# Optimization experiments

Measured on AMD Instinct MI355X. Metric: run time of the kernel, lower is better.

Reference implementation:

```python
import jax, jax.numpy as jnp
import numpy as np

U_NODES, V_NODES, N_EDGES = 100000, 50000, 2000000
F_DIM, G_DIM, H_DIM = 32, 32, 8
G_HIDDEN = (64, 32)
F_HIDDEN = (64, 32)
OUT_DIM = 1


def _linear_params(key, din, dout):
    kw, kb = jax.random.split(key)
    lim = 1.0 / np.sqrt(din)
    w = jax.random.uniform(kw, (din, dout), jnp.float32, -lim, lim)
    b = jax.random.uniform(kb, (dout,), jnp.float32, -lim, lim)
    return w, b


def setup_inputs() -> dict:
    key = jax.random.key(0)
    ks = jax.random.split(key, 10)
    u = jax.random.normal(ks[0], (U_NODES, F_DIM), jnp.float32)
    v = jax.random.normal(ks[1], (V_NODES, G_DIM), jnp.float32)
    e_vals = jax.random.normal(ks[2], (N_EDGES, H_DIM), jnp.float32)
    e_src = jax.random.randint(ks[3], (N_EDGES,), 0, V_NODES, jnp.int32)  # V-side index (indices[0])
    e_dst = jax.random.randint(ks[4], (N_EDGES,), 0, U_NODES, jnp.int32)  # U-side index (indices[1])
    g_w1, g_b1 = _linear_params(ks[5], F_DIM + G_DIM + H_DIM, G_HIDDEN[0])
    g_w2, g_b2 = _linear_params(ks[6], G_HIDDEN[0], G_HIDDEN[1])
    f_w1, f_b1 = _linear_params(ks[7], F_DIM + G_HIDDEN[1], F_HIDDEN[0])
    f_w2, f_b2 = _linear_params(ks[8], F_HIDDEN[0], F_HIDDEN[1])
    t_w, t_b = _linear_params(ks[9], F_HIDDEN[1], OUT_DIM)
    return {
        "u": u, "v": v, "e_vals": e_vals, "e_src": e_src, "e_dst": e_dst,
        "g_w1": g_w1, "g_b1": g_b1, "g_w2": g_w2, "g_b2": g_b2,
        "f_w1": f_w1, "f_b1": f_b1, "f_w2": f_w2, "f_b2": f_b2,
        "t_w": t_w, "t_b": t_b,
    }


def reference(u, v, e_vals, e_src, e_dst,
              g_w1, g_b1, g_w2, g_b2,
              f_w1, f_b1, f_w2, f_b2,
              t_w, t_b):
    # gather edge endpoint features -> g MLP (two Linear+ReLU layers)
    edge_in = jnp.concatenate([u[e_dst], v[e_src], e_vals], axis=-1)  # (E, F+G+H)
    h = jax.nn.relu(edge_in @ g_w1 + g_b1)
    h = jax.nn.relu(h @ g_w2 + g_b2)  # (E, D)
    # torch.sparse.sum over dim=-3 (V axis) == segment-sum by the U index
    agg = jax.ops.segment_sum(h, e_dst, num_segments=u.shape[0])  # (U, D)
    # f MLP on concat([u, agg])
    z = jax.nn.relu(jnp.concatenate([u, agg], axis=-1) @ f_w1 + f_b1)
    z = jax.nn.relu(z @ f_w2 + f_b2)
    # tail linear (no relu) + sigmoid
    return jax.nn.sigmoid(z @ t_w + t_b)  # (U, 1)
```

## Files before the change

kernel.cpp:

```cpp
#include <hip/hip_runtime.h>
#include <cstdint>
#include <cstddef>

#define U_NODES 100000
#define V_NODES 50000
#define N_EDGES 2000000
#define NSEG_CAP 25


typedef _Float16 f16x8 __attribute__((ext_vector_type(8)));
typedef _Float16 f16x2 __attribute__((ext_vector_type(2)));
typedef float    f32x4 __attribute__((ext_vector_type(4)));

__device__ __forceinline__ void load8f(const float* __restrict__ p, float* x) {
    const float4* p4 = reinterpret_cast<const float4*>(p);
    float4 a = p4[0], b = p4[1];
    x[0]=a.x; x[1]=a.y; x[2]=a.z; x[3]=a.w;
    x[4]=b.x; x[5]=b.y; x[6]=b.z; x[7]=b.w;
}

__device__ __forceinline__ void load32f(const float* __restrict__ p, float* x) {
    #pragma unroll
    for (int q = 0; q < 4; ++q) load8f(p + 8*q, x + 8*q);
}

__device__ __forceinline__ unsigned pack_bf16x2(float a, float b) {
    unsigned ua = __float_as_uint(a);
    ua = (ua + 0x7FFFu + ((ua >> 16) & 1u)) >> 16;
    unsigned ub = __float_as_uint(b);
    ub = (ub + 0x7FFFu + ((ub >> 16) & 1u)) & 0xFFFF0000u;
    return ua | ub;
}

__device__ __forceinline__ unsigned pk16(float a, float b) {
    union { f16x2 h; unsigned u; } c;
    c.h[0] = (_Float16)a; c.h[1] = (_Float16)b;
    return c.u;
}
__device__ __forceinline__ float f16lo(unsigned w) {
    union { unsigned short u; _Float16 h; } c; c.u = (unsigned short)(w & 0xFFFFu);
    return (float)c.h;
}
__device__ __forceinline__ float f16hi(unsigned w) {
    union { unsigned short u; _Float16 h; } c; c.u = (unsigned short)(w >> 16);
    return (float)c.h;
}
__device__ __forceinline__ f16x8 as_f16x8(uint4 x) {
    union { uint4 u; f16x8 h; } c; c.u = x; return c.h;
}

__device__ __forceinline__ float fdot2f(unsigned a, unsigned b, float c) {
#if defined(__has_builtin) && __has_builtin(__builtin_amdgcn_fdot2)
    union { unsigned u; f16x2 h; } ca, cb; ca.u = a; cb.u = b;
    return __builtin_amdgcn_fdot2(ca.h, cb.h, c, false);
#else
    return c + f16lo(a)*f16lo(b) + f16hi(a)*f16hi(b);
#endif
}


__global__ __launch_bounds__(256) void proj_u_kernel(
    const float* __restrict__ u, const float* __restrict__ g_w1,
    float* __restrict__ A)
{
    int n = blockIdx.x * 256 + threadIdx.x;
    if (n >= U_NODES) return;
    float x[32];
    load32f(u + (size_t)n * 32, x);
    float acc[64];
    #pragma unroll
    for (int j = 0; j < 64; ++j) acc[j] = 0.f;
    #pragma unroll
    for (int i = 0; i < 32; ++i) {
        #pragma unroll
        for (int j = 0; j < 64; ++j) acc[j] += x[i] * g_w1[i*64 + j];
    }
    float4* Ap = reinterpret_cast<float4*>(A + (size_t)n * 64);
    #pragma unroll
    for (int q = 0; q < 16; ++q)
        Ap[q] = make_float4(acc[4*q], acc[4*q+1], acc[4*q+2], acc[4*q+3]);
}

__global__ __launch_bounds__(256) void proj_v_kernel(
    const float* __restrict__ v, const float* __restrict__ g_w1,
    const float* __restrict__ g_b1, float* __restrict__ B)
{
    int n = blockIdx.x * 256 + threadIdx.x;
    if (n >= V_NODES) return;
    float x[32];
    load32f(v + (size_t)n * 32, x);
    float acc[64];
    #pragma unroll
    for (int j = 0; j < 64; ++j) acc[j] = g_b1[j];
    #pragma unroll
    for (int i = 0; i < 32; ++i) {
        #pragma unroll
        for (int j = 0; j < 64; ++j) acc[j] += x[i] * g_w1[(32+i)*64 + j];
    }
    float4* Bp = reinterpret_cast<float4*>(B + (size_t)n * 64);
    #pragma unroll
    for (int q = 0; q < 16; ++q)
        Bp[q] = make_float4(acc[4*q], acc[4*q+1], acc[4*q+2], acc[4*q+3]);
}


__global__ __launch_bounds__(256) void rank_kernel(
    const int* __restrict__ e_dst, int* __restrict__ deg, int* __restrict__ rank)
{
    int e = blockIdx.x * 256 + threadIdx.x;
    if (e >= N_EDGES) return;
    rank[e] = atomicAdd(&deg[e_dst[e]], 1);
}

__global__ __launch_bounds__(256) void scan_block_kernel(
    const int* __restrict__ deg, int* __restrict__ off, int* __restrict__ aux, int n)
{
    __shared__ int s[256];
    int tid = threadIdx.x;
    int i = blockIdx.x * 256 + tid;
    int x = (i < n) ? deg[i] : 0;
    s[tid] = x;
    __syncthreads();
    #pragma unroll
    for (int o = 1; o < 256; o <<= 1) {
        int t = (tid >= o) ? s[tid - o] : 0;
        __syncthreads();
        s[tid] += t;
        __syncthreads();
    }
    if (i < n) off[i + 1] = s[tid];
    if (tid == 255) aux[blockIdx.x] = s[255];
}

__global__ __launch_bounds__(512) void scan_aux_kernel(int* __restrict__ aux, int nA)
{
    __shared__ int s[512];
    int tid = threadIdx.x;
    int x = (tid < nA) ? aux[tid] : 0;
    s[tid] = x;
    __syncthreads();
    #pragma unroll
    for (int o = 1; o < 512; o <<= 1) {
        int t = (tid >= o) ? s[tid - o] : 0;
        __syncthreads();
        s[tid] += t;
        __syncthreads();
    }
    if (tid < nA) aux[tid] = s[tid] - x;
}

__global__ __launch_bounds__(256) void scan_add_kernel(
    int* __restrict__ off, const int* __restrict__ aux, int n)
{
    int i = blockIdx.x * 256 + threadIdx.x;
    if (i == 0) off[0] = 0;
    if (i < n) off[i + 1] += aux[i >> 8];
}

__global__ __launch_bounds__(256) void scatter_kernel(
    const int* __restrict__ e_dst, const int* __restrict__ off,
    const int* __restrict__ rank, int* __restrict__ sorted_eid)
{
    int e = blockIdx.x * 256 + threadIdx.x;
    if (e >= N_EDGES) return;
    int d = e_dst[e];
    sorted_eid[off[d] + rank[e]] = e;
}

__global__ __launch_bounds__(256) void permute_pack_kernel(
    const int* __restrict__ e_dst, const int* __restrict__ e_src,
    const int* __restrict__ rank, const int* __restrict__ off,
    const float* __restrict__ e_vals, unsigned* __restrict__ epk)
{
    int e = blockIdx.x * 256 + threadIdx.x;
    if (e >= N_EDGES) return;
    int d = e_dst[e];
    int pos = off[d] + rank[e];
    float ev[8];
    load8f(e_vals + (size_t)e * 8, ev);
    uint4 w0;
    w0.x = (unsigned)d;
    w0.y = (unsigned)e_src[e];
    w0.z = pk16(ev[0], ev[1]);
    w0.w = pk16(ev[2], ev[3]);
    uint2 w1;
    w1.x = pk16(ev[4], ev[5]);
    w1.y = pk16(ev[6], ev[7]);
    unsigned* dst = epk + (size_t)pos * 8;
    *reinterpret_cast<uint4*>(dst)     = w0;
    *reinterpret_cast<uint2*>(dst + 4) = w1;
}


__global__ __launch_bounds__(256) void edge_reg_kernel(
    const float* __restrict__ A, const float* __restrict__ B,
    const unsigned* __restrict__ epk,
    const float* __restrict__ g_w1, const float* __restrict__ g_w2,
    const float* __restrict__ g_b2, float* __restrict__ agg)
{
    __shared__ unsigned s_w2[32 * 33];
    __shared__ __align__(16) unsigned s_w1e[4 * 64];
    __shared__ int   s_d[256];
    __shared__ int   s_meta[4][64];
    __shared__ float s_agg[4][NSEG_CAP][33];
    __shared__ float pub_val[4][2][32];
    __shared__ int   pub_d[4][2];
    __shared__ int   pub_fl[4][2];
    __shared__ int   s_bprev, s_bnext;

    const int tid = threadIdx.x;
    const long bP = (long)blockIdx.x * 256;

    #pragma unroll
    for (int i = 0; i < 4; ++i) {
        int idx = tid + i * 256;
        int kp = idx >> 5, n = idx & 31;
        s_w2[kp * 33 + n] = pk16(g_w2[(2*kp)*32 + n], g_w2[(2*kp+1)*32 + n]);
    }
    {
        int i2 = tid >> 6, c = tid & 63;
        s_w1e[i2 * 64 + c] = pk16(g_w1[(64 + 2*i2)*64 + c], g_w1[(64 + 2*i2 + 1)*64 + c]);
    }
    if (tid == 0) {
        s_bprev = (bP > 0) ? (int)epk[(size_t)(bP - 1) * 8] : -2;
        s_bnext = (bP + 256 < (long)N_EDGES) ? (int)epk[(size_t)(bP + 256) * 8] : -2;
    }
    __syncthreads();

    const int wv   = tid >> 6;
    const int lane = tid & 63;
    const int lm   = lane & 15;
    const int lg   = lane >> 4;
    const long wP  = bP + wv * 64;

    int dM[4], sM[4];
    unsigned evp[4][4];
    #pragma unroll
    for (int mt = 0; mt < 4; ++mt) {
        long pe = wP + mt*16 + lm;
        if (pe < (long)N_EDGES) {
            const unsigned* ep = epk + (size_t)pe * 8;
            uint4 w0 = *reinterpret_cast<const uint4*>(ep);
            uint2 w1 = *reinterpret_cast<const uint2*>(ep + 4);
            dM[mt] = (int)w0.x; sM[mt] = (int)w0.y;
            evp[mt][0] = w0.z; evp[mt][1] = w0.w; evp[mt][2] = w1.x; evp[mt][3] = w1.y;
        } else {
            dM[mt] = -1; sM[mt] = 0;
            evp[mt][0] = evp[mt][1] = evp[mt][2] = evp[mt][3] = 0;
        }
    }
    if (lg == 0) {
        #pragma unroll
        for (int mt = 0; mt < 4; ++mt) s_d[wv*64 + mt*16 + lm] = dM[mt];
    }
    {
        float* z = &s_agg[wv][0][0];
        for (int i = lane; i < NSEG_CAP * 33; i += 64) z[i] = 0.f;
    }

    uint4 afr[4][2];
    #pragma unroll
    for (int kt = 0; kt < 2; ++kt) {
        float acc[4][8];
        #pragma unroll
        for (int mt = 0; mt < 4; ++mt) {
            if (dM[mt] >= 0) {
                const float4* Ap = reinterpret_cast<const float4*>(A + (size_t)dM[mt]*64 + kt*32 + lg*8);
                const float4* Bp = reinterpret_cast<const float4*>(B + (size_t)sM[mt]*64 + kt*32 + lg*8);
                float4 a0 = Ap[0], a1 = Ap[1], b0 = Bp[0], b1 = Bp[1];
                acc[mt][0] = a0.x + b0.x; acc[mt][1] = a0.y + b0.y;
                acc[mt][2] = a0.z + b0.z; acc[mt][3] = a0.w + b0.w;
                acc[mt][4] = a1.x + b1.x; acc[mt][5] = a1.y + b1.y;
                acc[mt][6] = a1.z + b1.z; acc[mt][7] = a1.w + b1.w;
            } else {
                #pragma unroll
                for (int j = 0; j < 8; ++j) acc[mt][j] = 0.f;
            }
        }
        #pragma unroll
        for (int i2 = 0; i2 < 4; ++i2) {
            uint4 wA = *reinterpret_cast<const uint4*>(&s_w1e[i2*64 + kt*32 + lg*8]);
            uint4 wB = *reinterpret_cast<const uint4*>(&s_w1e[i2*64 + kt*32 + lg*8 + 4]);
            unsigned wp0 = wA.x, wp1 = wA.y, wp2 = wA.z, wp3 = wA.w;
            unsigned wp4 = wB.x, wp5 = wB.y, wp6 = wB.z, wp7 = wB.w;
            #pragma unroll
            for (int mt = 0; mt < 4; ++mt) {
                unsigned e2 = evp[mt][i2];
                acc[mt][0] = fdot2f(e2, wp0, acc[mt][0]);
                acc[mt][1] = fdot2f(e2, wp1, acc[mt][1]);
                acc[mt][2] = fdot2f(e2, wp2, acc[mt][2]);
                acc[mt][3] = fdot2f(e2, wp3, acc[mt][3]);
                acc[mt][4] = fdot2f(e2, wp4, acc[mt][4]);
                acc[mt][5] = fdot2f(e2, wp5, acc[mt][5]);
                acc[mt][6] = fdot2f(e2, wp6, acc[mt][6]);
                acc[mt][7] = fdot2f(e2, wp7, acc[mt][7]);
            }
        }
        #pragma unroll
        for (int mt = 0; mt < 4; ++mt) {
            uint4 w;
            w.x = pk16(fmaxf(acc[mt][0], 0.f), fmaxf(acc[mt][1], 0.f));
            w.y = pk16(fmaxf(acc[mt][2], 0.f), fmaxf(acc[mt][3], 0.f));
            w.z = pk16(fmaxf(acc[mt][4], 0.f), fmaxf(acc[mt][5], 0.f));
            w.w = pk16(fmaxf(acc[mt][6], 0.f), fmaxf(acc[mt][7], 0.f));
            afr[mt][kt] = w;
        }
    }

    f32x4 mac[4][2];
    #pragma unroll
    for (int mt = 0; mt < 4; ++mt) {
        #pragma unroll
        for (int nt = 0; nt < 2; ++nt) {
            mac[mt][nt][0] = 0.f; mac[mt][nt][1] = 0.f;
            mac[mt][nt][2] = 0.f; mac[mt][nt][3] = 0.f;
        }
    }
    #pragma unroll
    for (int kt = 0; kt < 2; ++kt) {
        uint4 bf0, bf1;
        int kp = kt*16 + lg*4;
        bf0.x = s_w2[(kp+0)*33 + lm];      bf1.x = s_w2[(kp+0)*33 + 16 + lm];
        bf0.y = s_w2[(kp+1)*33 + lm];      bf1.y = s_w2[(kp+1)*33 + 16 + lm];
        bf0.z = s_w2[(kp+2)*33 + lm];      bf1.z = s_w2[(kp+2)*33 + 16 + lm];
        bf0.w = s_w2[(kp+3)*33 + lm];      bf1.w = s_w2[(kp+3)*33 + 16 + lm];
        f16x8 b0 = as_f16x8(bf0), b1 = as_f16x8(bf1);
        #pragma unroll
        for (int mt = 0; mt < 4; ++mt) {
            f16x8 a = as_f16x8(afr[mt][kt]);
            mac[mt][0] = __builtin_amdgcn_mfma_f32_16x16x32_f16(a, b0, mac[mt][0], 0, 0, 0);
            mac[mt][1] = __builtin_amdgcn_mfma_f32_16x16x32_f16(a, b1, mac[mt][1], 0, 0, 0);
        }
    }

    asm volatile("s_waitcnt lgkmcnt(0)" ::: "memory");

    int myd = s_d[wv*64 + lane];
    int prevd = (lane > 0) ? s_d[wv*64 + lane - 1] : -2;
    bool headb = (lane == 0) || (myd != prevd);
    unsigned long long mask = __ballot(headb);

    long remaining = (long)N_EDGES - wP;
    int validcnt = remaining >= 64 ? 64 : (remaining < 0 ? 0 : (int)remaining);
    unsigned long long vmask = (validcnt >= 64) ? ~0ull : ((1ull << validcnt) - 1ull);
    int nsegV = (int)__popcll(mask & vmask);

    if (headb && lane < validcnt) {
        int sg = (int)__popcll(mask & ((2ull << lane) - 1ull)) - 1;
        s_meta[wv][sg] = lane;
    }

    float b2a = g_b2[lm], b2b = g_b2[16 + lm];

    #pragma unroll
    for (int mt = 0; mt < 4; ++mt) {
        const int ebase = mt*16 + lg*4;
        float v0[4], v1[4];
        #pragma unroll
        for (int r = 0; r < 4; ++r) {
            v0[r] = fmaxf(mac[mt][0][r] + b2a, 0.f);
            v1[r] = fmaxf(mac[mt][1][r] + b2b, 0.f);
        }
        float cs0 = v0[0], cs1 = v1[0];
        int rstart = 0;
        #pragma unroll
        for (int r = 1; r <= 4; ++r) {
            bool cut = (r == 4) || (((mask >> (ebase + r)) & 1ull) != 0);
            if (cut) {
                int e0 = ebase + rstart;
                int dd = s_d[wv*64 + e0];
                if (dd >= 0) {
                    int sg = (int)__popcll(mask & ((2ull << e0) - 1ull)) - 1;
                    if (sg < NSEG_CAP) {
                        atomicAdd(&s_agg[wv][sg][lm], cs0);
                        atomicAdd(&s_agg[wv][sg][16 + lm], cs1);
                    } else {
                        atomicAdd(agg + (size_t)dd*32 + lm, cs0);
                        atomicAdd(agg + (size_t)dd*32 + 16 + lm, cs1);
                    }
                }
                if (r < 4) { rstart = r; cs0 = v0[r]; cs1 = v1[r]; }
            } else {
                cs0 += v0[r]; cs1 += v1[r];
            }
        }
    }

    asm volatile("s_waitcnt lgkmcnt(0)" ::: "memory");

    int nI = (nsegV - 1 < NSEG_CAP ? nsegV - 1 : NSEG_CAP) - 1;
    for (int it = lane; it < nI * 32; it += 64) {
        int sg = 1 + (it >> 5);
        int c  = it & 31;
        int dd = s_d[wv*64 + s_meta[wv][sg]];
        agg[(size_t)dd*32 + c] = s_agg[wv][sg][c];
    }

    if (lane < 32) {
        int c = lane;
        if (nsegV >= 1) {
            pub_val[wv][0][c] = s_agg[wv][0][c];
            if (c == 0) { pub_d[wv][0] = s_d[wv*64]; pub_fl[wv][0] = 0; }
        } else if (c == 0) { pub_d[wv][0] = -3; pub_fl[wv][0] = 0; }
    } else {
        int c = lane - 32;
        if (nsegV >= 2) {
            int sL = nsegV - 1;
            if (sL < NSEG_CAP) {
                pub_val[wv][1][c] = s_agg[wv][sL][c];
                if (c == 0) { pub_d[wv][1] = s_d[wv*64 + s_meta[wv][sL]]; pub_fl[wv][1] = 0; }
            } else {
                pub_val[wv][1][c] = 0.f;
                if (c == 0) { pub_d[wv][1] = s_d[wv*64 + s_meta[wv][sL]]; pub_fl[wv][1] = 1; }
            }
        } else if (c == 0) { pub_d[wv][1] = -3; pub_fl[wv][1] = 0; }
    }
    __syncthreads();

    if (tid < 32) {
        const int c = tid;
        int firstV = -1, lastV = -1;
        #pragma unroll
        for (int k = 0; k < 8; ++k) {
            int dk = pub_d[k >> 1][k & 1];
            if (dk >= 0) { if (firstV < 0) firstV = k; lastV = k; }
        }
        int k = firstV;
        while (firstV >= 0 && k <= lastV) {
            int dk = pub_d[k >> 1][k & 1];
            if (dk < 0) { ++k; continue; }
            int d0 = dk; int kst = k;
            float s = 0.f; int atm = 0;
            while (k <= lastV) {
                int d2 = pub_d[k >> 1][k & 1];
                if (d2 == d0) {
                    s += pub_val[k >> 1][k & 1][c];
                    atm |= pub_fl[k >> 1][k & 1];
                    ++k;
                } else if (d2 < 0) { ++k; }
                else break;
            }
            bool lo = (kst == firstV) && (s_bprev == d0);
            bool ro = (k > lastV) && (s_bnext == d0);
            float* dst = agg + (size_t)d0*32 + c;
            if (lo || ro || atm) atomicAdd(dst, s);
            else *dst = s;
        }
    }
}


template <bool HAS_A>
__global__ __launch_bounds__(256) void edge_mfma_kernel(
    const float* __restrict__ A, const float* __restrict__ B,
    const float* __restrict__ u, const unsigned* __restrict__ epk,
    const float* __restrict__ g_w1, const float* __restrict__ g_w2,
    const float* __restrict__ g_b2, float* __restrict__ agg)
{
    __shared__ unsigned s_h1[256 * 36];
    __shared__ unsigned s_w2[32 * 33];
    __shared__ int s_d[256];
    __shared__ int s_heads[256];
    __shared__ int s_cnt, s_prevd, s_nextd;

    const int tid = threadIdx.x;
    const long p = (long)blockIdx.x * 256 + tid;

    if (tid == 0) {
        s_cnt = 0;
        long pprev = (long)blockIdx.x * 256 - 1;
        s_prevd = (pprev < 0) ? -2 : (int)epk[(size_t)pprev * 8];
        long pnext = (long)blockIdx.x * 256 + 256;
        s_nextd = (pnext >= N_EDGES) ? -2 : (int)epk[(size_t)pnext * 8];
    }
    #pragma unroll
    for (int i = 0; i < 4; ++i) {
        int idx = tid + i * 256;
        int kp = idx >> 5, n = idx & 31;
        s_w2[kp * 33 + n] = pk16(g_w2[(2*kp)*32 + n], g_w2[(2*kp+1)*32 + n]);
    }

    int d = -1;
    if (p < N_EDGES) {
        const unsigned* ep = epk + (size_t)p * 8;
        uint4 w0 = *reinterpret_cast<const uint4*>(ep);
        uint2 w1 = *reinterpret_cast<const uint2*>(ep + 4);
        d = (int)w0.x;
        int s = (int)w0.y;

        float h1[64];
        if constexpr (HAS_A) {
            const float4* Ap = reinterpret_cast<const float4*>(A + (size_t)d * 64);
            #pragma unroll
            for (int q = 0; q < 16; ++q) {
                float4 a = Ap[q];
                h1[4*q+0] = a.x; h1[4*q+1] = a.y; h1[4*q+2] = a.z; h1[4*q+3] = a.w;
            }
        } else {
            #pragma unroll
            for (int j = 0; j < 64; ++j) h1[j] = 0.f;
            float x[32];
            load32f(u + (size_t)d * 32, x);
            #pragma unroll
            for (int i = 0; i < 32; ++i) {
                #pragma unroll
                for (int j = 0; j < 64; ++j) h1[j] += x[i] * g_w1[i*64 + j];
            }
        }
        {
            const float4* Bp = reinterpret_cast<const float4*>(B + (size_t)s * 64);
            #pragma unroll
            for (int q = 0; q < 16; ++q) {
                float4 b = Bp[q];
                h1[4*q+0] += b.x; h1[4*q+1] += b.y; h1[4*q+2] += b.z; h1[4*q+3] += b.w;
            }
        }
        float ev[8];
        ev[0]=f16lo(w0.z); ev[1]=f16hi(w0.z); ev[2]=f16lo(w0.w); ev[3]=f16hi(w0.w);
        ev[4]=f16lo(w1.x); ev[5]=f16hi(w1.x); ev[6]=f16lo(w1.y); ev[7]=f16hi(w1.y);
        #pragma unroll
        for (int i = 0; i < 8; ++i) {
            #pragma unroll
            for (int j = 0; j < 64; ++j) h1[j] += ev[i] * g_w1[(64+i)*64 + j];
        }
        #pragma unroll
        for (int j = 0; j < 64; ++j) h1[j] = fmaxf(h1[j], 0.f);

        #pragma unroll
        for (int q = 0; q < 8; ++q) {
            uint4 w;
            w.x = pk16(h1[8*q+0], h1[8*q+1]);
            w.y = pk16(h1[8*q+2], h1[8*q+3]);
            w.z = pk16(h1[8*q+4], h1[8*q+5]);
            w.w = pk16(h1[8*q+6], h1[8*q+7]);
            *reinterpret_cast<uint4*>(&s_h1[tid*36 + 4*q]) = w;
        }
    }
    s_d[tid] = d;
    __syncthreads();

    if (p < N_EDGES) {
        int prevd = (tid == 0) ? s_prevd : s_d[tid - 1];
        bool true_head = (prevd != d);
        bool is_head = (tid == 0) || true_head;
        if (is_head) {
            int idx = atomicAdd(&s_cnt, 1);
            s_heads[idx] = tid | (true_head ? 0x10000 : 0);
        }
    }

    const int lane = tid & 63;
    const int wb   = (tid >> 6) * 64;
    const int lg   = lane >> 4;
    const int lm   = lane & 15;

    f32x4 acc[4][2];
    #pragma unroll
    for (int mt = 0; mt < 4; ++mt) {
        #pragma unroll
        for (int nt = 0; nt < 2; ++nt) {
            acc[mt][nt][0] = 0.f; acc[mt][nt][1] = 0.f;
            acc[mt][nt][2] = 0.f; acc[mt][nt][3] = 0.f;
        }
    }
    #pragma unroll
    for (int kt = 0; kt < 2; ++kt) {
        uint4 bf0, bf1;
        int kp = kt*16 + lg*4;
        bf0.x = s_w2[(kp+0)*33 + lm];      bf1.x = s_w2[(kp+0)*33 + 16 + lm];
        bf0.y = s_w2[(kp+1)*33 + lm];      bf1.y = s_w2[(kp+1)*33 + 16 + lm];
        bf0.z = s_w2[(kp+2)*33 + lm];      bf1.z = s_w2[(kp+2)*33 + 16 + lm];
        bf0.w = s_w2[(kp+3)*33 + lm];      bf1.w = s_w2[(kp+3)*33 + 16 + lm];
        f16x8 b0 = as_f16x8(bf0), b1 = as_f16x8(bf1);
        #pragma unroll
        for (int mt = 0; mt < 4; ++mt) {
            uint4 av = *reinterpret_cast<const uint4*>(
                &s_h1[(wb + mt*16 + lm)*36 + kt*16 + lg*4]);
            f16x8 a = as_f16x8(av);
            acc[mt][0] = __builtin_amdgcn_mfma_f32_16x16x32_f16(a, b0, acc[mt][0], 0, 0, 0);
            acc[mt][1] = __builtin_amdgcn_mfma_f32_16x16x32_f16(a, b1, acc[mt][1], 0, 0, 0);
        }
    }
    float b2a = g_b2[lm];
    float b2b = g_b2[16 + lm];
    __syncthreads();

    float* h2f = reinterpret_cast<float*>(s_h1);
    #pragma unroll
    for (int mt = 0; mt < 4; ++mt) {
        #pragma unroll
        for (int r = 0; r < 4; ++r) {
            int row = wb + mt*16 + lg*4 + r;
            h2f[row*36 + lm]      = fmaxf(acc[mt][0][r] + b2a, 0.f);
            h2f[row*36 + 16 + lm] = fmaxf(acc[mt][1][r] + b2b, 0.f);
        }
    }
    __syncthreads();

    const int nseg = s_cnt;
    const int next_d = s_nextd;
    for (int w = tid; w < nseg * 16; w += 256) {
        int seg = w >> 4, cp = w & 15;
        int ent = s_heads[seg];
        int h = ent & 0xFFFF;
        bool thead = (ent & 0x10000) != 0;
        int dd = s_d[h];
        float s0 = 0.f, s1 = 0.f;
        int r = h;
        while (r < 256 && s_d[r] == dd) {
            s0 += h2f[r*36 + 2*cp];
            s1 += h2f[r*36 + 2*cp + 1];
            ++r;
        }
        bool end_complete = (r < 256) || (next_d != dd);
        float* dst = agg + (size_t)dd * 32 + 2 * cp;
        if (thead && end_complete) {
            *reinterpret_cast<float2*>(dst) = make_float2(s0, s1);
        } else {
            atomicAdd(dst + 0, s0);
            atomicAdd(dst + 1, s1);
        }
    }
}


template <bool HAS_A, bool HAS_B>
__global__ __launch_bounds__(256) void edge_sorted_kernel(
    const float* __restrict__ A, const float* __restrict__ B,
    const float* __restrict__ u, const float* __restrict__ v,
    const float* __restrict__ e_vals, const int* __restrict__ e_src,
    const int* __restrict__ e_dst, const int* __restrict__ seid,
    const float* __restrict__ g_w1, const float* __restrict__ g_b1,
    const float* __restrict__ g_w2, const float* __restrict__ g_b2,
    float* __restrict__ agg)
{
    __shared__ unsigned lds_h[256][17];
    __shared__ int lds_d[256];
    __shared__ int lds_heads[256];
    __shared__ int lds_cnt;
    __shared__ int lds_prev_d, lds_next_d;

    const int tid = threadIdx.x;
    const long p = (long)blockIdx.x * 256 + tid;

    if (tid == 0) {
        lds_cnt = 0;
        long pprev = (long)blockIdx.x * 256 - 1;
        lds_prev_d = (pprev < 0) ? -2 : e_dst[seid[pprev]];
        long pnext = (long)blockIdx.x * 256 + 256;
        lds_next_d = (pnext >= N_EDGES) ? -2 : e_dst[seid[pnext]];
    }

    int d = -1;
    if (p < N_EDGES) {
        int eid = seid[p];
        d = e_dst[eid];
        int s = e_src[eid];

        float h1[64];
        if constexpr (HAS_A) {
            const float4* Ap = reinterpret_cast<const float4*>(A + (size_t)d * 64);
            #pragma unroll
            for (int q = 0; q < 16; ++q) {
                float4 a = Ap[q];
                h1[4*q+0] = a.x; h1[4*q+1] = a.y; h1[4*q+2] = a.z; h1[4*q+3] = a.w;
            }
        } else {
            #pragma unroll
            for (int j = 0; j < 64; ++j) h1[j] = 0.f;
            float x[32];
            load32f(u + (size_t)d * 32, x);
            #pragma unroll
            for (int i = 0; i < 32; ++i) {
                #pragma unroll
                for (int j = 0; j < 64; ++j) h1[j] += x[i] * g_w1[i*64 + j];
            }
        }
        if constexpr (HAS_B) {
            const float4* Bp = reinterpret_cast<const float4*>(B + (size_t)s * 64);
            #pragma unroll
            for (int q = 0; q < 16; ++q) {
                float4 b = Bp[q];
                h1[4*q+0] += b.x; h1[4*q+1] += b.y; h1[4*q+2] += b.z; h1[4*q+3] += b.w;
            }
        } else {
            #pragma unroll
            for (int j = 0; j < 64; ++j) h1[j] += g_b1[j];
            float x[32];
            load32f(v + (size_t)s * 32, x);
            #pragma unroll
            for (int i = 0; i < 32; ++i) {
                #pragma unroll
                for (int j = 0; j < 64; ++j) h1[j] += x[i] * g_w1[(32+i)*64 + j];
            }
        }
        float ev[8];
        load8f(e_vals + (size_t)eid * 8, ev);
        #pragma unroll
        for (int i = 0; i < 8; ++i) {
            #pragma unroll
            for (int j = 0; j < 64; ++j) h1[j] += ev[i] * g_w1[(64+i)*64 + j];
        }
        #pragma unroll
        for (int j = 0; j < 64; ++j) h1[j] = fmaxf(h1[j], 0.f);

        float h2[32];
        #pragma unroll
        for (int k = 0; k < 32; ++k) h2[k] = g_b2[k];
        #pragma unroll
        for (int i = 0; i < 64; ++i) {
            #pragma unroll
            for (int k = 0; k < 32; ++k) h2[k] += h1[i] * g_w2[i*32 + k];
        }
        #pragma unroll
        for (int cp = 0; cp < 16; ++cp)
            lds_h[tid][cp] = pack_bf16x2(fmaxf(h2[2*cp], 0.f), fmaxf(h2[2*cp+1], 0.f));
    }
    lds_d[tid] = d;
    __syncthreads();

    if (p < N_EDGES) {
        int prevd = (tid == 0) ? lds_prev_d : lds_d[tid - 1];
        bool true_head = (prevd != d);
        bool is_head = (tid == 0) || true_head;
        if (is_head) {
            int idx = atomicAdd(&lds_cnt, 1);
            lds_heads[idx] = tid | (true_head ? 0x10000 : 0);
        }
    }
    __syncthreads();

    const int nseg = lds_cnt;
    const int next_d = lds_next_d;
    for (int w = tid; w < nseg * 16; w += 256) {
        int seg = w >> 4, cp = w & 15;
        int ent = lds_heads[seg];
        int h = ent & 0xFFFF;
        bool thead = (ent & 0x10000) != 0;
        int dd = lds_d[h];
        float s0 = 0.f, s1 = 0.f;
        int r = h;
        while (r < 256 && lds_d[r] == dd) {
            unsigned x = lds_h[r][cp];
            s0 += __uint_as_float(x << 16);
            s1 += __uint_as_float(x & 0xFFFF0000u);
            ++r;
        }
        bool end_complete = (r < 256) || (next_d != dd);
        float* dst = agg + (size_t)dd * 32 + 2 * cp;
        if (thead && end_complete) {
            *reinterpret_cast<float2*>(dst) = make_float2(s0, s1);
        } else {
            atomicAdd(dst + 0, s0);
            atomicAdd(dst + 1, s1);
        }
    }
}


__global__ __launch_bounds__(256) void node_kernel(
    const float* __restrict__ u, const float* __restrict__ agg,
    const float* __restrict__ f_w1, const float* __restrict__ f_b1,
    const float* __restrict__ f_w2, const float* __restrict__ f_b2,
    const float* __restrict__ t_w, const float* __restrict__ t_b,
    float* __restrict__ out)
{
    int n = blockIdx.x * 256 + threadIdx.x;
    if (n >= U_NODES) return;
    float x[64];
    load32f(u   + (size_t)n * 32, x);
    load32f(agg + (size_t)n * 32, x + 32);
    float z1[64];
    #pragma unroll
    for (int j = 0; j < 64; ++j) z1[j] = f_b1[j];
    #pragma unroll
    for (int i = 0; i < 64; ++i) {
        #pragma unroll
        for (int j = 0; j < 64; ++j) z1[j] += x[i] * f_w1[i*64 + j];
    }
    #pragma unroll
    for (int j = 0; j < 64; ++j) z1[j] = fmaxf(z1[j], 0.f);
    float z2[32];
    #pragma unroll
    for (int k = 0; k < 32; ++k) z2[k] = f_b2[k];
    #pragma unroll
    for (int j = 0; j < 64; ++j) {
        #pragma unroll
        for (int k = 0; k < 32; ++k) z2[k] += z1[j] * f_w2[j*32 + k];
    }
    #pragma unroll
    for (int k = 0; k < 32; ++k) z2[k] = fmaxf(z2[k], 0.f);
    float o = t_b[0];
    #pragma unroll
    for (int k = 0; k < 32; ++k) o += z2[k] * t_w[k];
    out[n] = 1.f / (1.f + expf(-o));
}


__global__ __launch_bounds__(256) void edge_direct_kernel(
    const float* __restrict__ u, const float* __restrict__ v,
    const float* __restrict__ e_vals, const int* __restrict__ e_src,
    const int* __restrict__ e_dst, const float* __restrict__ g_w1,
    const float* __restrict__ g_b1, const float* __restrict__ g_w2,
    const float* __restrict__ g_b2, float* __restrict__ agg)
{
    int e = blockIdx.x * 256 + threadIdx.x;
    if (e >= N_EDGES) return;
    int d = e_dst[e];
    int s = e_src[e];
    float x[72];
    load32f(u + (size_t)d * 32, x);
    load32f(v + (size_t)s * 32, x + 32);
    load8f(e_vals + (size_t)e * 8, x + 64);
    float h1[64];
    #pragma unroll
    for (int j = 0; j < 64; ++j) h1[j] = g_b1[j];
    #pragma unroll
    for (int i = 0; i < 72; ++i) {
        #pragma unroll
        for (int j = 0; j < 64; ++j) h1[j] += x[i] * g_w1[i*64 + j];
    }
    #pragma unroll
    for (int j = 0; j < 64; ++j) h1[j] = fmaxf(h1[j], 0.f);
    float acc2[32];
    #pragma unroll
    for (int k = 0; k < 32; ++k) acc2[k] = g_b2[k];
    #pragma unroll
    for (int i = 0; i < 64; ++i) {
        #pragma unroll
        for (int k = 0; k < 32; ++k) acc2[k] += h1[i] * g_w2[i*32 + k];
    }
    float* aggp = agg + (size_t)d * 32;
    #pragma unroll
    for (int k = 0; k < 32; ++k) atomicAdd(aggp + k, fmaxf(acc2[k], 0.f));
}


static inline size_t align256(size_t x) { return (x + 255) & ~(size_t)255; }

extern "C" void kernel_launch(void* const* d_in, const int* in_sizes, int n_in,
                              void* d_out, int out_size, void* d_ws, size_t ws_size,
                              hipStream_t stream) {
    const float* u      = (const float*)d_in[0];
    const float* v      = (const float*)d_in[1];
    const float* e_vals = (const float*)d_in[2];
    const int*   e_src  = (const int*)  d_in[3];
    const int*   e_dst  = (const int*)  d_in[4];
    const float* g_w1   = (const float*)d_in[5];
    const float* g_b1   = (const float*)d_in[6];
    const float* g_w2   = (const float*)d_in[7];
    const float* g_b2   = (const float*)d_in[8];
    const float* f_w1   = (const float*)d_in[9];
    const float* f_b1   = (const float*)d_in[10];
    const float* f_w2   = (const float*)d_in[11];
    const float* f_b2   = (const float*)d_in[12];
    const float* t_w    = (const float*)d_in[13];
    const float* t_b    = (const float*)d_in[14];
    float* out = (float*)d_out;

    char* wsc = (char*)d_ws;
    const int nChunks = (U_NODES + 255) / 256;
    const int eBlocks = (N_EDGES + 255) / 256;

    const size_t degB  = align256((size_t)U_NODES * 4);
    const size_t offB  = align256((size_t)(U_NODES + 1) * 4);
    const size_t auxB  = align256((size_t)nChunks * 4);
    const size_t aggB  = align256((size_t)U_NODES * 32 * 4);
    const size_t e4B   = align256((size_t)N_EDGES * 4);
    const size_t epkB  = align256((size_t)N_EDGES * 32);
    const size_t bB    = align256((size_t)V_NODES * 64 * 4);
    const size_t aB    = align256((size_t)U_NODES * 64 * 4);

    size_t o = 0;
    size_t oDeg = o; o += degB;
    size_t oOff = o; o += offB;
    size_t oAux = o; o += auxB;
    size_t oAgg = o; o += aggB;
    size_t baseNeed = o;

    size_t oEp = o;  o += epkB;
    size_t oBn = o;  o += bB;
    size_t needT2r = o + e4B;
    size_t oAn = o;  o += aB;
    size_t needT1 = o;

    size_t o3 = baseNeed;
    size_t oSeid = o3; o3 += e4B;
    size_t needT4 = o3 + e4B;
    size_t oB3 = o3;   o3 += bB;
    size_t oA3 = o3;   o3 += aB;
    size_t needT3 = o3;

    int* deg   = (int*)(wsc + oDeg);
    int* off   = (int*)(wsc + oOff);
    int* aux   = (int*)(wsc + oAux);
    float* agg = (float*)(wsc + oAgg);

    if (ws_size >= needT2r) {
        const bool hasA = (ws_size >= needT1);
        unsigned* epk = (unsigned*)(wsc + oEp);
        float* B   = (float*)(wsc + oBn);
        float* A   = hasA ? (float*)(wsc + oAn) : nullptr;
        int* rank  = hasA ? (int*)A : (int*)(wsc + oAn);

        hipMemsetAsync(deg, 0, (size_t)U_NODES * 4, stream);
        hipMemsetAsync(agg, 0, (size_t)U_NODES * 32 * 4, stream);

        rank_kernel<<<eBlocks, 256, 0, stream>>>(e_dst, deg, rank);
        scan_block_kernel<<<nChunks, 256, 0, stream>>>(deg, off, aux, U_NODES);
        scan_aux_kernel<<<1, 512, 0, stream>>>(aux, nChunks);
        scan_add_kernel<<<nChunks, 256, 0, stream>>>(off, aux, U_NODES);
        permute_pack_kernel<<<eBlocks, 256, 0, stream>>>(e_dst, e_src, rank, off,
                                                         e_vals, epk);
        proj_v_kernel<<<(V_NODES + 255) / 256, 256, 0, stream>>>(v, g_w1, g_b1, B);
        if (hasA) {
            proj_u_kernel<<<(U_NODES + 255) / 256, 256, 0, stream>>>(u, g_w1, A);
            edge_reg_kernel<<<eBlocks, 256, 0, stream>>>(
                A, B, epk, g_w1, g_w2, g_b2, agg);
        } else {
            edge_mfma_kernel<false><<<eBlocks, 256, 0, stream>>>(
                nullptr, B, u, epk, g_w1, g_w2, g_b2, agg);
        }
        node_kernel<<<(U_NODES + 255) / 256, 256, 0, stream>>>(
            u, agg, f_w1, f_b1, f_w2, f_b2, t_w, t_b, out);
    } else if (ws_size >= needT4) {
        const bool hasAB = (ws_size >= needT3);
        int* seid = (int*)(wsc + oSeid);
        float* B = hasAB ? (float*)(wsc + oB3) : nullptr;
        float* A = hasAB ? (float*)(wsc + oA3) : nullptr;
        int* rank = hasAB ? (int*)A : (int*)(wsc + oSeid + e4B);

        hipMemsetAsync(deg, 0, (size_t)U_NODES * 4, stream);
        hipMemsetAsync(agg, 0, (size_t)U_NODES * 32 * 4, stream);

        rank_kernel<<<eBlocks, 256, 0, stream>>>(e_dst, deg, rank);
        scan_block_kernel<<<nChunks, 256, 0, stream>>>(deg, off, aux, U_NODES);
        scan_aux_kernel<<<1, 512, 0, stream>>>(aux, nChunks);
        scan_add_kernel<<<nChunks, 256, 0, stream>>>(off, aux, U_NODES);
        scatter_kernel<<<eBlocks, 256, 0, stream>>>(e_dst, off, rank, seid);

        if (hasAB) {
            proj_v_kernel<<<(V_NODES + 255) / 256, 256, 0, stream>>>(v, g_w1, g_b1, B);
            proj_u_kernel<<<(U_NODES + 255) / 256, 256, 0, stream>>>(u, g_w1, A);
            edge_sorted_kernel<true, true><<<eBlocks, 256, 0, stream>>>(
                A, B, u, v, e_vals, e_src, e_dst, seid, g_w1, g_b1, g_w2, g_b2, agg);
        } else {
            edge_sorted_kernel<false, false><<<eBlocks, 256, 0, stream>>>(
                nullptr, nullptr, u, v, e_vals, e_src, e_dst, seid,
                g_w1, g_b1, g_w2, g_b2, agg);
        }
        node_kernel<<<(U_NODES + 255) / 256, 256, 0, stream>>>(
            u, agg, f_w1, f_b1, f_w2, f_b2, t_w, t_b, out);
    } else {
        float* agg0 = (float*)wsc;
        hipMemsetAsync(agg0, 0, (size_t)U_NODES * 32 * 4, stream);
        edge_direct_kernel<<<eBlocks, 256, 0, stream>>>(
            u, v, e_vals, e_src, e_dst, g_w1, g_b1, g_w2, g_b2, agg0);
        node_kernel<<<(U_NODES + 255) / 256, 256, 0, stream>>>(
            u, agg0, f_w1, f_b1, f_w2, f_b2, t_w, t_b, out);
    }
}
```

Measured before the change: 495.3 us.

## Replace per-wave LDS-atomic segment reduction with block-wide head-list segmented sum

The edge kernel's aggregation is rebuilt. The old scheme used per-wave shared-memory atomics, a segment cap, and a cross-wave publish and merge step. Now each block writes its second-layer activations to shared memory as bf16, builds a list of segment heads over all 256 edges, and gives each segment 16 threads that sum its rows serially. A segment is written to global memory with a plain store unless it crosses a block boundary, in which case atomics are used. This removes most LDS and global atomics and the serial merge by a single thread. It adds bf16 rounding before the summation and a serial per-segment loop.

```diff
diff --git a/kernel.cpp b/kernel.cpp
--- a/kernel.cpp
+++ b/kernel.cpp
@@ -5,7 +5,6 @@
 #define U_NODES 100000
 #define V_NODES 50000
 #define N_EDGES 2000000
-#define NSEG_CAP 25
 
 
 typedef _Float16 f16x8 __attribute__((ext_vector_type(8)));
@@ -30,6 +29,10 @@
     unsigned ub = __float_as_uint(b);
     ub = (ub + 0x7FFFu + ((ub >> 16) & 1u)) & 0xFFFF0000u;
     return ua | ub;
+}
+__device__ __forceinline__ unsigned short bf16_1(float a) {
+    unsigned ua = __float_as_uint(a);
+    return (unsigned short)((ua + 0x7FFFu + ((ua >> 16) & 1u)) >> 16);
 }
 
 __device__ __forceinline__ unsigned pk16(float a, float b) {
@@ -192,7 +195,7 @@
 }
 
 
-__global__ __launch_bounds__(256) void edge_reg_kernel(
+__global__ __launch_bounds__(256) void edge_frag_kernel(
     const float* __restrict__ A, const float* __restrict__ B,
     const unsigned* __restrict__ epk,
     const float* __restrict__ g_w1, const float* __restrict__ g_w2,
@@ -200,13 +203,10 @@
 {
     __shared__ unsigned s_w2[32 * 33];
     __shared__ __align__(16) unsigned s_w1e[4 * 64];
-    __shared__ int   s_d[256];
-    __shared__ int   s_meta[4][64];
-    __shared__ float s_agg[4][NSEG_CAP][33];
-    __shared__ float pub_val[4][2][32];
-    __shared__ int   pub_d[4][2];
-    __shared__ int   pub_fl[4][2];
-    __shared__ int   s_bprev, s_bnext;
+    __shared__ unsigned s_h2[256 * 17];
+    __shared__ int s_d[256];
+    __shared__ int s_heads[256];
+    __shared__ int s_cnt, s_prevd, s_nextd;
 
     const int tid = threadIdx.x;
     const long bP = (long)blockIdx.x * 256;
@@ -222,10 +222,10 @@
         s_w1e[i2 * 64 + c] = pk16(g_w1[(64 + 2*i2)*64 + c], g_w1[(64 + 2*i2 + 1)*64 + c]);
     }
     if (tid == 0) {
-        s_bprev = (bP > 0) ? (int)epk[(size_t)(bP - 1) * 8] : -2;
-        s_bnext = (bP + 256 < (long)N_EDGES) ? (int)epk[(size_t)(bP + 256) * 8] : -2;
-    }
-    __syncthreads();
+        s_cnt = 0;
+        s_prevd = (bP > 0) ? (int)epk[(size_t)(bP - 1) * 8] : -2;
+        s_nextd = (bP + 256 < (long)N_EDGES) ? (int)epk[(size_t)(bP + 256) * 8] : -2;
+    }
 
     const int wv   = tid >> 6;
     const int lane = tid & 63;
@@ -248,14 +248,19 @@
             dM[mt] = -1; sM[mt] = 0;
             evp[mt][0] = evp[mt][1] = evp[mt][2] = evp[mt][3] = 0;
         }
-    }
-    if (lg == 0) {
-        #pragma unroll
-        for (int mt = 0; mt < 4; ++mt) s_d[wv*64 + mt*16 + lm] = dM[mt];
-    }
-    {
-        float* z = &s_agg[wv][0][0];
-        for (int i = lane; i < NSEG_CAP * 33; i += 64) z[i] = 0.f;
+        if (lg == 0) s_d[wv*64 + mt*16 + lm] = dM[mt];
+    }
+    __syncthreads();
+
+    if (bP + tid < (long)N_EDGES) {
+        int d_me  = s_d[tid];
+        int prevd = (tid == 0) ? s_prevd : s_d[tid - 1];
+        bool true_head = (prevd != d_me);
+        bool is_head = (tid == 0) || true_head;
+        if (is_head) {
+            int idx = atomicAdd(&s_cnt, 1);
+            s_heads[idx] = tid | (true_head ? 0x10000 : 0);
+        }
     }
 
     uint4 afr[4][2];
@@ -281,19 +286,17 @@
         for (int i2 = 0; i2 < 4; ++i2) {
             uint4 wA = *reinterpret_cast<const uint4*>(&s_w1e[i2*64 + kt*32 + lg*8]);
             uint4 wB = *reinterpret_cast<const uint4*>(&s_w1e[i2*64 + kt*32 + lg*8 + 4]);
-            unsigned wp0 = wA.x, wp1 = wA.y, wp2 = wA.z, wp3 = wA.w;
-            unsigned wp4 = wB.x, wp5 = wB.y, wp6 = wB.z, wp7 = wB.w;
             #pragma unroll
             for (int mt = 0; mt < 4; ++mt) {
                 unsigned e2 = evp[mt][i2];
-                acc[mt][0] = fdot2f(e2, wp0, acc[mt][0]);
-                acc[mt][1] = fdot2f(e2, wp1, acc[mt][1]);
-                acc[mt][2] = fdot2f(e2, wp2, acc[mt][2]);
-                acc[mt][3] = fdot2f(e2, wp3, acc[mt][3]);
-                acc[mt][4] = fdot2f(e2, wp4, acc[mt][4]);
-                acc[mt][5] = fdot2f(e2, wp5, acc[mt][5]);
-                acc[mt][6] = fdot2f(e2, wp6, acc[mt][6]);
-                acc[mt][7] = fdot2f(e2, wp7, acc[mt][7]);
+                acc[mt][0] = fdot2f(e2, wA.x, acc[mt][0]);
+                acc[mt][1] = fdot2f(e2, wA.y, acc[mt][1]);
+                acc[mt][2] = fdot2f(e2, wA.z, acc[mt][2]);
+                acc[mt][3] = fdot2f(e2, wA.w, acc[mt][3]);
+                acc[mt][4] = fdot2f(e2, wB.x, acc[mt][4]);
+                acc[mt][5] = fdot2f(e2, wB.y, acc[mt][5]);
+                acc[mt][6] = fdot2f(e2, wB.z, acc[mt][6]);
+                acc[mt][7] = fdot2f(e2, wB.w, acc[mt][7]);
             }
         }
         #pragma unroll
@@ -333,118 +336,42 @@
         }
     }
 
-    asm volatile("s_waitcnt lgkmcnt(0)" ::: "memory");
-
-    int myd = s_d[wv*64 + lane];
-    int prevd = (lane > 0) ? s_d[wv*64 + lane - 1] : -2;
-    bool headb = (lane == 0) || (myd != prevd);
-    unsigned long long mask = __ballot(headb);
-
-    long remaining = (long)N_EDGES - wP;
-    int validcnt = remaining >= 64 ? 64 : (remaining < 0 ? 0 : (int)remaining);
-    unsigned long long vmask = (validcnt >= 64) ? ~0ull : ((1ull << validcnt) - 1ull);
-    int nsegV = (int)__popcll(mask & vmask);
-
-    if (headb && lane < validcnt) {
-        int sg = (int)__popcll(mask & ((2ull << lane) - 1ull)) - 1;
-        s_meta[wv][sg] = lane;
-    }
-
     float b2a = g_b2[lm], b2b = g_b2[16 + lm];
-
+    unsigned short* h2s = reinterpret_cast<unsigned short*>(s_h2);
     #pragma unroll
     for (int mt = 0; mt < 4; ++mt) {
-        const int ebase = mt*16 + lg*4;
-        float v0[4], v1[4];
         #pragma unroll
         for (int r = 0; r < 4; ++r) {
-            v0[r] = fmaxf(mac[mt][0][r] + b2a, 0.f);
-            v1[r] = fmaxf(mac[mt][1][r] + b2b, 0.f);
-        }
-        float cs0 = v0[0], cs1 = v1[0];
-        int rstart = 0;
-        #pragma unroll
-        for (int r = 1; r <= 4; ++r) {
-            bool cut = (r == 4) || (((mask >> (ebase + r)) & 1ull) != 0);
-            if (cut) {
-                int e0 = ebase + rstart;
-                int dd = s_d[wv*64 + e0];
-                if (dd >= 0) {
-                    int sg = (int)__popcll(mask & ((2ull << e0) - 1ull)) - 1;
-                    if (sg < NSEG_CAP) {
-                        atomicAdd(&s_agg[wv][sg][lm], cs0);
-                        atomicAdd(&s_agg[wv][sg][16 + lm], cs1);
-                    } else {
-                        atomicAdd(agg + (size_t)dd*32 + lm, cs0);
-                        atomicAdd(agg + (size_t)dd*32 + 16 + lm, cs1);
-                    }
-                }
-                if (r < 4) { rstart = r; cs0 = v0[r]; cs1 = v1[r]; }
-            } else {
-                cs0 += v0[r]; cs1 += v1[r];
-            }
-        }
-    }
-
-    asm volatile("s_waitcnt lgkmcnt(0)" ::: "memory");
-
-    int nI = (nsegV - 1 < NSEG_CAP ? nsegV - 1 : NSEG_CAP) - 1;
-    for (int it = lane; it < nI * 32; it += 64) {
-        int sg = 1 + (it >> 5);
-        int c  = it & 31;
-        int dd = s_d[wv*64 + s_meta[wv][sg]];
-        agg[(size_t)dd*32 + c] = s_agg[wv][sg][c];
-    }
-
-    if (lane < 32) {
-        int c = lane;
-        if (nsegV >= 1) {
-            pub_val[wv][0][c] = s_agg[wv][0][c];
-            if (c == 0) { pub_d[wv][0] = s_d[wv*64]; pub_fl[wv][0] = 0; }
-        } else if (c == 0) { pub_d[wv][0] = -3; pub_fl[wv][0] = 0; }
-    } else {
-        int c = lane - 32;
-        if (nsegV >= 2) {
-            int sL = nsegV - 1;
-            if (sL < NSEG_CAP) {
-                pub_val[wv][1][c] = s_agg[wv][sL][c];
-                if (c == 0) { pub_d[wv][1] = s_d[wv*64 + s_meta[wv][sL]]; pub_fl[wv][1] = 0; }
-            } else {
-                pub_val[wv][1][c] = 0.f;
-                if (c == 0) { pub_d[wv][1] = s_d[wv*64 + s_meta[wv][sL]]; pub_fl[wv][1] = 1; }
-            }
-        } else if (c == 0) { pub_d[wv][1] = -3; pub_fl[wv][1] = 0; }
+            int edge = wv*64 + mt*16 + lg*4 + r;
+            h2s[edge*34 + lm]      = bf16_1(fmaxf(mac[mt][0][r] + b2a, 0.f));
+            h2s[edge*34 + 16 + lm] = bf16_1(fmaxf(mac[mt][1][r] + b2b, 0.f));
+        }
     }
     __syncthreads();
 
-    if (tid < 32) {
-        const int c = tid;
-        int firstV = -1, lastV = -1;
-        #pragma unroll
-        for (int k = 0; k < 8; ++k) {
-            int dk = pub_d[k >> 1][k & 1];
-            if (dk >= 0) { if (firstV < 0) firstV = k; lastV = k; }
-        }
-        int k = firstV;
-        while (firstV >= 0 && k <= lastV) {
-            int dk = pub_d[k >> 1][k & 1];
-            if (dk < 0) { ++k; continue; }
-            int d0 = dk; int kst = k;
-            float s = 0.f; int atm = 0;
-            while (k <= lastV) {
-                int d2 = pub_d[k >> 1][k & 1];
-                if (d2 == d0) {
-                    s += pub_val[k >> 1][k & 1][c];
-                    atm |= pub_fl[k >> 1][k & 1];
-                    ++k;
-                } else if (d2 < 0) { ++k; }
-                else break;
-            }
-            bool lo = (kst == firstV) && (s_bprev == d0);
-            bool ro = (k > lastV) && (s_bnext == d0);
-            float* dst = agg + (size_t)d0*32 + c;
-            if (lo || ro || atm) atomicAdd(dst, s);
-            else *dst = s;
+    const int nseg = s_cnt;
+    const int next_d = s_nextd;
+    for (int w = tid; w < nseg * 16; w += 256) {
+        int seg = w >> 4, cp = w & 15;
+        int ent = s_heads[seg];
+        int h = ent & 0xFFFF;
+        bool thead = (ent & 0x10000) != 0;
+        int dd = s_d[h];
+        float s0 = 0.f, s1 = 0.f;
+        int r = h;
+        while (r < 256 && s_d[r] == dd) {
+            unsigned x = s_h2[r*17 + cp];
+            s0 += __uint_as_float(x << 16);
+            s1 += __uint_as_float(x & 0xFFFF0000u);
+            ++r;
+        }
+        bool end_complete = (r < 256) || (next_d != dd);
+        float* dst = agg + (size_t)dd * 32 + 2 * cp;
+        if (thead && end_complete) {
+            *reinterpret_cast<float2*>(dst) = make_float2(s0, s1);
+        } else {
+            atomicAdd(dst + 0, s0);
+            atomicAdd(dst + 1, s1);
         }
     }
 }
@@ -915,7 +842,7 @@
         proj_v_kernel<<<(V_NODES + 255) / 256, 256, 0, stream>>>(v, g_w1, g_b1, B);
         if (hasA) {
             proj_u_kernel<<<(U_NODES + 255) / 256, 256, 0, stream>>>(u, g_w1, A);
-            edge_reg_kernel<<<eBlocks, 256, 0, stream>>>(
+            edge_frag_kernel<<<eBlocks, 256, 0, stream>>>(
                 A, B, epk, g_w1, g_w2, g_b2, agg);
         } else {
             edge_mfma_kernel<false><<<eBlocks, 256, 0, stream>>>(
```

After: 424.4 us. -14.3%, faster.
